# Optimization experiments

Measured on AMD Instinct MI355X. Metric: run time of the kernel, lower is better.

Reference implementation:

```python
import jax, jax.numpy as jnp
import numpy as np

DIM = 512

def setup_inputs() -> dict:
    key = jax.random.key(0)
    ks = jax.random.split(key, 8)
    B, T, S, D = 4, 128, 512, DIM
    scale = 1.0 / np.sqrt(D)
    return {
        "inp": jax.random.normal(ks[0], (B, T, D), jnp.float32),
        "context": jax.random.normal(ks[1], (B, S, D), jnp.float32),
        # linear_query: Linear(D, D, bias=True)
        "Wq": jax.random.normal(ks[2], (D, D), jnp.float32) * scale,
        "bq": jax.random.normal(ks[3], (D,), jnp.float32) * scale,
        # linear_context: Linear(D, D, bias=False)
        "Wc": jax.random.normal(ks[4], (D, D), jnp.float32) * scale,
        # v: Linear(D, 1, bias=False)
        "v": jax.random.normal(ks[5], (D,), jnp.float32) * scale,
        # linear_out: Linear(2D, D, bias=True)
        "Wout": jax.random.normal(ks[6], (D, 2 * D), jnp.float32) * scale,
        "bout": jax.random.normal(ks[7], (D,), jnp.float32) * scale,
    }

def reference(inp, context, Wq, bq, Wc, v, Wout, bout):
    # inp: (B,T,D) target queries; context: (B,S,D) source states
    wq = jnp.einsum('btd,ed->bte', inp, Wq) + bq          # (B,T,D)
    uh = jnp.einsum('bsd,ed->bse', context, Wc)            # (B,S,D)
    # additive (Bahdanau) score: v^T tanh(Wq q_t + Wc h_s)
    wquh = jnp.tanh(wq[:, :, None, :] + uh[:, None, :, :])  # (B,T,S,D)
    align = jnp.einsum('btsd,d->bts', wquh, v)             # (B,T,S)
    align_vectors = jax.nn.softmax(align, axis=-1)          # softmax over src_len
    c = jnp.einsum('bts,bsd->btd', align_vectors, context)  # context vector
    concat_c = jnp.concatenate([c, inp], axis=-1)           # (B,T,2D)
    attn_h = jnp.einsum('btf,ef->bte', concat_c, Wout) + bout  # (B,T,D)
    return attn_h, align_vectors
```

## Files before the change

### kernel.cpp

```cpp
#include <hip/hip_runtime.h>
#include <hip/hip_bf16.h>
#include <math.h>


typedef __attribute__((ext_vector_type(8))) short short8;
typedef __attribute__((ext_vector_type(4))) float f32x4;
typedef unsigned short ushort_t;

static __device__ __forceinline__ unsigned short f2bf(float x) {
    union { __hip_bfloat16 h; unsigned short u; } c;
    c.h = __float2bfloat16(x);
    return c.u;
}
static __device__ __forceinline__ int bf2x(float lo, float hi) {
    return (int)(((unsigned)f2bf(hi) << 16) | (unsigned)f2bf(lo));
}

template<bool BF>
static __device__ __forceinline__ void load16(const void* base, size_t elemoff,
                                              int4& r0, int4& r1) {
    if (BF) {
        const int4* p = (const int4*)((const ushort_t*)base + elemoff);
        r0 = p[0]; r1 = p[1];
    } else {
        const float4* p = (const float4*)((const float*)base + elemoff);
        float4 a = p[0], b = p[1], c = p[2], d = p[3];
        r0.x = bf2x(a.x, a.y); r0.y = bf2x(a.z, a.w);
        r0.z = bf2x(b.x, b.y); r0.w = bf2x(b.z, b.w);
        r1.x = bf2x(c.x, c.y); r1.y = bf2x(c.z, c.w);
        r1.z = bf2x(d.x, d.y); r1.w = bf2x(d.z, d.w);
    }
}

template<bool A_BF, bool W_BF, int EPI>
static __device__ __forceinline__ void gemm_body(
    ushort_t* As, ushort_t* Ws,
    const void* A, const void* W, const float* bias,
    void* Cv, int K, int lda, int ldw, int ldc, int bm, int bn)
{
    const int tid = threadIdx.x;
    const int wave = tid >> 6, lane = tid & 63;
    const int mh = (wave & 1) * 32, nh = (wave >> 1) * 32;
    const int quad = lane >> 4, l16 = lane & 15;
    const int srow = tid >> 2, schunk = tid & 3;

    const size_t aoff = (size_t)(bm + srow) * lda + schunk * 16;
    const size_t woff = (size_t)(bn + srow) * ldw + schunk * 16;
    int4* AsW = (int4*)&As[srow * 72 + schunk * 16];
    int4* WsW = (int4*)&Ws[srow * 72 + schunk * 16];

    f32x4 acc00 = {0.f, 0.f, 0.f, 0.f}, acc01 = acc00, acc10 = acc00, acc11 = acc00;

    int4 a0r, a1r, w0r, w1r;
    load16<A_BF>(A, aoff, a0r, a1r);
    load16<W_BF>(W, woff, w0r, w1r);

    for (int k0 = 0; k0 < K; k0 += 64) {
        AsW[0] = a0r; AsW[1] = a1r;
        WsW[0] = w0r; WsW[1] = w1r;
        __syncthreads();
        if (k0 + 64 < K) {
            load16<A_BF>(A, aoff + k0 + 64, a0r, a1r);
            load16<W_BF>(W, woff + k0 + 64, w0r, w1r);
        }
        #pragma unroll
        for (int kk = 0; kk < 64; kk += 32) {
            short8 a0 = *(const short8*)&As[(mh + l16) * 72 + kk + quad * 8];
            short8 a1 = *(const short8*)&As[(mh + 16 + l16) * 72 + kk + quad * 8];
            short8 b0 = *(const short8*)&Ws[(nh + l16) * 72 + kk + quad * 8];
            short8 b1 = *(const short8*)&Ws[(nh + 16 + l16) * 72 + kk + quad * 8];
            acc00 = __builtin_amdgcn_mfma_f32_16x16x32_bf16(a0, b0, acc00, 0, 0, 0);
            acc01 = __builtin_amdgcn_mfma_f32_16x16x32_bf16(a0, b1, acc01, 0, 0, 0);
            acc10 = __builtin_amdgcn_mfma_f32_16x16x32_bf16(a1, b0, acc10, 0, 0, 0);
            acc11 = __builtin_amdgcn_mfma_f32_16x16x32_bf16(a1, b1, acc11, 0, 0, 0);
        }
        __syncthreads();
    }

    const int col0 = bn + nh + l16;
    const int col1 = col0 + 16;
    float bias0 = bias ? bias[col0] : 0.f;
    float bias1 = bias ? bias[col1] : 0.f;

    f32x4 accs[2][2] = {{acc00, acc01}, {acc10, acc11}};
    #pragma unroll
    for (int mt = 0; mt < 2; ++mt) {
        #pragma unroll
        for (int r = 0; r < 4; ++r) {
            int row = bm + mh + mt * 16 + quad * 4 + r;
            size_t rowoff = (size_t)row * ldc;
            float v0 = accs[mt][0][r] + bias0;
            float v1 = accs[mt][1][r] + bias1;
            if (EPI == 1) { v0 = __expf(2.f * v0); v1 = __expf(2.f * v1); }
            if (EPI == 2) {
                ushort_t* C = (ushort_t*)Cv;
                C[rowoff + col0] = f2bf(v0);
                C[rowoff + col1] = f2bf(v1);
            } else {
                float* C = (float*)Cv;
                C[rowoff + col0] = v0;
                C[rowoff + col1] = v1;
            }
        }
    }
}

__global__ __launch_bounds__(256) void fused_front(
    const float* __restrict__ inp, const float* __restrict__ ctx,
    const float* __restrict__ Wq, const float* __restrict__ bq,
    const float* __restrict__ Wc, const float* __restrict__ Wout,
    const float* __restrict__ bout,
    float* __restrict__ Ew, float* __restrict__ Eu, float* __restrict__ Y0,
    ushort_t* __restrict__ GT)
{
    __shared__ ushort_t As[64 * 72];
    __shared__ ushort_t Ws[64 * 72];
    const int bid = blockIdx.x;

    if (bid < 64) {
        gemm_body<false, false, 1>(As, Ws, inp, Wq, bq, Ew,
                                   512, 512, 512, 512, (bid & 7) * 64, (bid >> 3) * 64);
    } else if (bid < 320) {
        int i = bid - 64;
        gemm_body<false, false, 1>(As, Ws, ctx, Wc, nullptr, Eu,
                                   512, 512, 512, 512, (i & 31) * 64, (i >> 5) * 64);
    } else if (bid < 576) {
        int i = bid - 320;
        int b = i >> 6, j = i & 63;
        gemm_body<false, false, 2>(As, Ws, Wout, ctx + (size_t)b * 262144, nullptr,
                                   GT + (size_t)b * 262144,
                                   512, 1024, 512, 512, (j & 7) * 64, (j >> 3) * 64);
    } else {
        int i = bid - 576;
        gemm_body<false, false, 0>(As, Ws, inp, Wout + 512, bout, Y0,
                                   512, 512, 1024, 512, (i & 7) * 64, (i >> 3) * 64);
    }
}

__global__ __launch_bounds__(256) void align_kernel(
    const float* __restrict__ Ew, const float* __restrict__ Eu,
    const float* __restrict__ v, float* __restrict__ out)
{
    const int lane = threadIdx.x & 63, wave = threadIdx.x >> 6;
    const int b = blockIdx.z;
    const int t0 = blockIdx.y * 8 + wave * 2;
    const int s0 = blockIdx.x * 8;

    const float* w0p = Ew + (((size_t)(b * 128 + t0)) << 9);
    const float* w1p = w0p + 512;
    const float* up  = Eu + (((size_t)(b * 512 + s0)) << 9);

    float acc0[8], acc1[8];
    #pragma unroll
    for (int j = 0; j < 8; ++j) { acc0[j] = 0.f; acc1[j] = 0.f; }
    float vsum = 0.f;

    for (int k0 = 0; k0 < 512; k0 += 64) {
        float vk = v[k0 + lane];
        vsum += vk;
        float w0 = w0p[k0 + lane];
        float w1 = w1p[k0 + lane];
        #pragma unroll
        for (int j = 0; j < 8; ++j) {
            float u = up[((size_t)j << 9) + k0 + lane];
            float d0 = fmaf(w0, u, 1.f);
            float d1 = fmaf(w1, u, 1.f);
            float r0 = __builtin_amdgcn_rcpf(d0);
            float r1 = __builtin_amdgcn_rcpf(d1);
            acc0[j] = fmaf(vk, r0, acc0[j]);
            acc1[j] = fmaf(vk, r1, acc1[j]);
        }
    }

    float V = vsum;
    #pragma unroll
    for (int off = 32; off; off >>= 1) V += __shfl_xor(V, off, 64);

    float r0 = 0.f, r1 = 0.f;
    #pragma unroll
    for (int j = 0; j < 8; ++j) {
        float a = acc0[j], c = acc1[j];
        #pragma unroll
        for (int off = 32; off; off >>= 1) {
            a += __shfl_xor(a, off, 64);
            c += __shfl_xor(c, off, 64);
        }
        if (lane == j) { r0 = fmaf(-2.f, a, V); r1 = fmaf(-2.f, c, V); }
    }
    if (lane < 8) {
        size_t o = (((size_t)(b * 128 + t0)) << 9) + s0 + lane;
        out[o] = r0;
        out[o + 512] = r1;
    }
}

__global__ __launch_bounds__(256) void gemm_att(
    const float* __restrict__ Sraw, const ushort_t* __restrict__ GT,
    const float* __restrict__ Y0, float* __restrict__ attn,
    float* __restrict__ alignv)
{
    __shared__ ushort_t As[64 * 72];
    __shared__ ushort_t Ws[64 * 72];
    const int tid = threadIdx.x;
    const int b = blockIdx.z;
    const int bm = blockIdx.x * 64;
    const int bn = blockIdx.y * 64;
    const int wave = tid >> 6, lane = tid & 63;
    const int mh = (wave & 1) * 32, nh = (wave >> 1) * 32;
    const int quad = lane >> 4, l16 = lane & 15;
    const int srow = tid >> 2, schunk = tid & 3;

    const float* Srow = Sraw + (((size_t)(b * 128 + bm + srow)) << 9);

    const float4* qv = (const float4*)(Srow + schunk * 128);
    float mloc = -3.4e38f;
    #pragma unroll
    for (int i = 0; i < 32; ++i) {
        float4 x = qv[i];
        mloc = fmaxf(mloc, fmaxf(fmaxf(x.x, x.y), fmaxf(x.z, x.w)));
    }
    mloc = fmaxf(mloc, __shfl_xor(mloc, 1, 64));
    mloc = fmaxf(mloc, __shfl_xor(mloc, 2, 64));
    float ssum = 0.f;
    #pragma unroll
    for (int i = 0; i < 32; ++i) {
        float4 x = qv[i];
        ssum += __expf(x.x - mloc) + __expf(x.y - mloc)
              + __expf(x.z - mloc) + __expf(x.w - mloc);
    }
    ssum += __shfl_xor(ssum, 1, 64);
    ssum += __shfl_xor(ssum, 2, 64);
    const float rinv = __builtin_amdgcn_rcpf(ssum);

    const bool wr = (blockIdx.y == 0);
    float* arow = alignv + (((size_t)(b * 128 + bm + srow)) << 9);
    const ushort_t* GTb = GT + (size_t)b * 262144;
    const size_t woff = (size_t)(bn + srow) * 512 + schunk * 16;
    int4* AsW = (int4*)&As[srow * 72 + schunk * 16];
    int4* WsW = (int4*)&Ws[srow * 72 + schunk * 16];

    f32x4 acc00 = {0.f, 0.f, 0.f, 0.f}, acc01 = acc00, acc10 = acc00, acc11 = acc00;

    for (int k0 = 0; k0 < 512; k0 += 64) {
        const float4* ap = (const float4*)(Srow + k0 + schunk * 16);
        float4 x0 = ap[0], x1 = ap[1], x2 = ap[2], x3 = ap[3];
        float4 p0, p1, p2, p3;
        p0.x = __expf(x0.x - mloc) * rinv; p0.y = __expf(x0.y - mloc) * rinv;
        p0.z = __expf(x0.z - mloc) * rinv; p0.w = __expf(x0.w - mloc) * rinv;
        p1.x = __expf(x1.x - mloc) * rinv; p1.y = __expf(x1.y - mloc) * rinv;
        p1.z = __expf(x1.z - mloc) * rinv; p1.w = __expf(x1.w - mloc) * rinv;
        p2.x = __expf(x2.x - mloc) * rinv; p2.y = __expf(x2.y - mloc) * rinv;
        p2.z = __expf(x2.z - mloc) * rinv; p2.w = __expf(x2.w - mloc) * rinv;
        p3.x = __expf(x3.x - mloc) * rinv; p3.y = __expf(x3.y - mloc) * rinv;
        p3.z = __expf(x3.z - mloc) * rinv; p3.w = __expf(x3.w - mloc) * rinv;
        int4 w0r, w1r;
        load16<true>(GTb, woff + k0, w0r, w1r);
        if (wr) {
            float4* d = (float4*)(arow + k0 + schunk * 16);
            d[0] = p0; d[1] = p1; d[2] = p2; d[3] = p3;
        }
        int4 a0r, a1r;
        a0r.x = bf2x(p0.x, p0.y); a0r.y = bf2x(p0.z, p0.w);
        a0r.z = bf2x(p1.x, p1.y); a0r.w = bf2x(p1.z, p1.w);
        a1r.x = bf2x(p2.x, p2.y); a1r.y = bf2x(p2.z, p2.w);
        a1r.z = bf2x(p3.x, p3.y); a1r.w = bf2x(p3.z, p3.w);
        __syncthreads();
        AsW[0] = a0r; AsW[1] = a1r;
        WsW[0] = w0r; WsW[1] = w1r;
        __syncthreads();
        #pragma unroll
        for (int kk = 0; kk < 64; kk += 32) {
            short8 a0 = *(const short8*)&As[(mh + l16) * 72 + kk + quad * 8];
            short8 a1 = *(const short8*)&As[(mh + 16 + l16) * 72 + kk + quad * 8];
            short8 b0 = *(const short8*)&Ws[(nh + l16) * 72 + kk + quad * 8];
            short8 b1 = *(const short8*)&Ws[(nh + 16 + l16) * 72 + kk + quad * 8];
            acc00 = __builtin_amdgcn_mfma_f32_16x16x32_bf16(a0, b0, acc00, 0, 0, 0);
            acc01 = __builtin_amdgcn_mfma_f32_16x16x32_bf16(a0, b1, acc01, 0, 0, 0);
            acc10 = __builtin_amdgcn_mfma_f32_16x16x32_bf16(a1, b0, acc10, 0, 0, 0);
            acc11 = __builtin_amdgcn_mfma_f32_16x16x32_bf16(a1, b1, acc11, 0, 0, 0);
        }
    }

    const int col0 = bn + nh + l16;
    const int col1 = col0 + 16;
    f32x4 accs[2][2] = {{acc00, acc01}, {acc10, acc11}};
    #pragma unroll
    for (int mt = 0; mt < 2; ++mt) {
        #pragma unroll
        for (int r = 0; r < 4; ++r) {
            size_t rowoff = (size_t)(b * 128 + bm + mh + mt * 16 + quad * 4 + r) << 9;
            attn[rowoff + col0] = accs[mt][0][r] + Y0[rowoff + col0];
            attn[rowoff + col1] = accs[mt][1][r] + Y0[rowoff + col1];
        }
    }
}

extern "C" void kernel_launch(void* const* d_in, const int* in_sizes, int n_in,
                              void* d_out, int out_size, void* d_ws, size_t ws_size,
                              hipStream_t stream)
{
    const float* inp  = (const float*)d_in[0];
    const float* ctx  = (const float*)d_in[1];
    const float* Wq   = (const float*)d_in[2];
    const float* bq   = (const float*)d_in[3];
    const float* Wc   = (const float*)d_in[4];
    const float* v    = (const float*)d_in[5];
    const float* Wout = (const float*)d_in[6];
    const float* bout = (const float*)d_in[7];

    float* out   = (float*)d_out;
    float* attn  = out;
    float* align = out + 262144;

    float* ws = (float*)d_ws;
    float* Ew   = ws;
    float* Eu   = ws + 262144;
    float* Y0   = ws + 1310720;
    float* Sraw = ws + 1572864;
    ushort_t* GT = (ushort_t*)(ws + 1835008);

    fused_front<<<dim3(640), 256, 0, stream>>>(inp, ctx, Wq, bq, Wc, Wout, bout,
                                               Ew, Eu, Y0, GT);
    align_kernel<<<dim3(64, 16, 4), 256, 0, stream>>>(Ew, Eu, v, Sraw);
    gemm_att<<<dim3(2, 8, 4), 256, 0, stream>>>(Sraw, GT, Y0, attn, align);
}
```

Measured before the change: 127.6 us.

## Fuse three kernels into one persistent kernel with grid barriers

Result: slower. 294.4 us (+130.6%).

```diff
diff --git a/kernel.cpp b/kernel.cpp
--- a/kernel.cpp
+++ b/kernel.cpp
@@ -56,6 +56,7 @@
     load16<W_BF>(W, woff, w0r, w1r);
 
     for (int k0 = 0; k0 < K; k0 += 64) {
+        __syncthreads();
         AsW[0] = a0r; AsW[1] = a1r;
         WsW[0] = w0r; WsW[1] = w1r;
         __syncthreads();
@@ -74,7 +75,6 @@
             acc10 = __builtin_amdgcn_mfma_f32_16x16x32_bf16(a1, b0, acc10, 0, 0, 0);
             acc11 = __builtin_amdgcn_mfma_f32_16x16x32_bf16(a1, b1, acc11, 0, 0, 0);
         }
-        __syncthreads();
     }
 
     const int col0 = bn + nh + l16;
@@ -105,46 +105,41 @@
     }
 }
 
-__global__ __launch_bounds__(256) void fused_front(
-    const float* __restrict__ inp, const float* __restrict__ ctx,
-    const float* __restrict__ Wq, const float* __restrict__ bq,
-    const float* __restrict__ Wc, const float* __restrict__ Wout,
-    const float* __restrict__ bout,
-    float* __restrict__ Ew, float* __restrict__ Eu, float* __restrict__ Y0,
-    ushort_t* __restrict__ GT)
-{
-    __shared__ ushort_t As[64 * 72];
-    __shared__ ushort_t Ws[64 * 72];
-    const int bid = blockIdx.x;
-
-    if (bid < 64) {
+static __device__ __forceinline__ void front_tile(
+    int t, ushort_t* As, ushort_t* Ws,
+    const float* inp, const float* ctx, const float* Wq, const float* bq,
+    const float* Wc, const float* Wout, const float* bout,
+    float* Ew, float* Eu, float* Y0, ushort_t* GT)
+{
+    if (t < 64) {
         gemm_body<false, false, 1>(As, Ws, inp, Wq, bq, Ew,
-                                   512, 512, 512, 512, (bid & 7) * 64, (bid >> 3) * 64);
-    } else if (bid < 320) {
-        int i = bid - 64;
+                                   512, 512, 512, 512, (t & 7) * 64, (t >> 3) * 64);
+    } else if (t < 320) {
+        int i = t - 64;
         gemm_body<false, false, 1>(As, Ws, ctx, Wc, nullptr, Eu,
                                    512, 512, 512, 512, (i & 31) * 64, (i >> 5) * 64);
-    } else if (bid < 576) {
-        int i = bid - 320;
+    } else if (t < 576) {
+        int i = t - 320;
         int b = i >> 6, j = i & 63;
         gemm_body<false, false, 2>(As, Ws, Wout, ctx + (size_t)b * 262144, nullptr,
                                    GT + (size_t)b * 262144,
                                    512, 1024, 512, 512, (j & 7) * 64, (j >> 3) * 64);
     } else {
-        int i = bid - 576;
+        int i = t - 576;
         gemm_body<false, false, 0>(As, Ws, inp, Wout + 512, bout, Y0,
                                    512, 512, 1024, 512, (i & 7) * 64, (i >> 3) * 64);
     }
 }
 
-__global__ __launch_bounds__(256) void align_kernel(
-    const float* __restrict__ Ew, const float* __restrict__ Eu,
-    const float* __restrict__ v, float* __restrict__ out)
+static __device__ __forceinline__ void align_tile(
+    int idx, const float* Ew, const float* Eu, const float* v, float* out)
 {
     const int lane = threadIdx.x & 63, wave = threadIdx.x >> 6;
-    const int b = blockIdx.z;
-    const int t0 = blockIdx.y * 8 + wave * 2;
-    const int s0 = blockIdx.x * 8;
+    const int sx = idx & 63;
+    const int ty = (idx >> 6) & 15;
+    const int b  = idx >> 10;
+    const int t0 = ty * 8 + wave * 2;
+    const int s0 = sx * 8;
 
     const float* w0p = Ew + (((size_t)(b * 128 + t0)) << 9);
     const float* w1p = w0p + 512;
@@ -194,17 +189,14 @@
     }
 }
 
-__global__ __launch_bounds__(256) void gemm_att(
-    const float* __restrict__ Sraw, const ushort_t* __restrict__ GT,
-    const float* __restrict__ Y0, float* __restrict__ attn,
-    float* __restrict__ alignv)
-{
-    __shared__ ushort_t As[64 * 72];
-    __shared__ ushort_t Ws[64 * 72];
+static __device__ __forceinline__ void att_tile(
+    int idx, ushort_t* As, ushort_t* Ws,
+    const float* Sraw, const ushort_t* GT, const float* Y0,
+    float* attn, float* alignv)
+{
+    const int bx = idx & 1, by = (idx >> 1) & 7, b = idx >> 4;
     const int tid = threadIdx.x;
-    const int b = blockIdx.z;
-    const int bm = blockIdx.x * 64;
-    const int bn = blockIdx.y * 64;
+    const int bm = bx * 64, bn = by * 64;
     const int wave = tid >> 6, lane = tid & 63;
     const int mh = (wave & 1) * 32, nh = (wave >> 1) * 32;
     const int quad = lane >> 4, l16 = lane & 15;
@@ -232,7 +224,7 @@
     ssum += __shfl_xor(ssum, 2, 64);
     const float rinv = __builtin_amdgcn_rcpf(ssum);
 
-    const bool wr = (blockIdx.y == 0);
+    const bool wr = (by == 0);
     float* arow = alignv + (((size_t)(b * 128 + bm + srow)) << 9);
     const ushort_t* GTb = GT + (size_t)b * 262144;
     const size_t woff = (size_t)(bn + srow) * 512 + schunk * 16;
@@ -295,6 +287,45 @@
     }
 }
 
+static __device__ __forceinline__ void grid_barrier(int* bar, int target) {
+    __syncthreads();
+    if (threadIdx.x == 0) {
+        __threadfence();
+        __hip_atomic_fetch_add(bar, 1, __ATOMIC_ACQ_REL, __HIP_MEMORY_SCOPE_AGENT);
+        while (__hip_atomic_load(bar, __ATOMIC_ACQUIRE, __HIP_MEMORY_SCOPE_AGENT) < target)
+            __builtin_amdgcn_s_sleep(2);
+        __threadfence();
+    }
+    __syncthreads();
+}
+
+__global__ __launch_bounds__(256, 4) void mega(
+    const float* __restrict__ inp, const float* __restrict__ ctx,
+    const float* __restrict__ Wq, const float* __restrict__ bq,
+    const float* __restrict__ Wc, const float* __restrict__ v,
+    const float* __restrict__ Wout, const float* __restrict__ bout,
+    float* __restrict__ Ew, float* __restrict__ Eu, float* __restrict__ Y0,
+    ushort_t* __restrict__ GT, float* __restrict__ Sraw,
+    float* __restrict__ attn, float* __restrict__ alignv, int* bar)
+{
+    __shared__ ushort_t As[64 * 72];
+    __shared__ ushort_t Ws[64 * 72];
+    const int nblk = gridDim.x;
+
+    for (int t = blockIdx.x; t < 640; t += nblk)
+        front_tile(t, As, Ws, inp, ctx, Wq, bq, Wc, Wout, bout, Ew, Eu, Y0, GT);
+
+    grid_barrier(bar, nblk);
+
+    for (int i = blockIdx.x; i < 4096; i += nblk)
+        align_tile(i, Ew, Eu, v, Sraw);
+
+    grid_barrier(bar, 2 * nblk);
+
+    for (int i = blockIdx.x; i < 64; i += nblk)
+        att_tile(i, As, Ws, Sraw, GT, Y0, attn, alignv);
+}
+
 extern "C" void kernel_launch(void* const* d_in, const int* in_sizes, int n_in,
                               void* d_out, int out_size, void* d_ws, size_t ws_size,
                               hipStream_t stream)
@@ -308,9 +339,9 @@
     const float* Wout = (const float*)d_in[6];
     const float* bout = (const float*)d_in[7];
 
-    float* out   = (float*)d_out;
-    float* attn  = out;
-    float* align = out + 262144;
+    float* out    = (float*)d_out;
+    float* attn   = out;
+    float* alignv = out + 262144;
 
     float* ws = (float*)d_ws;
     float* Ew   = ws;
@@ -318,9 +349,16 @@
     float* Y0   = ws + 1310720;
     float* Sraw = ws + 1572864;
     ushort_t* GT = (ushort_t*)(ws + 1835008);
-
-    fused_front<<<dim3(640), 256, 0, stream>>>(inp, ctx, Wq, bq, Wc, Wout, bout,
-                                               Ew, Eu, Y0, GT);
-    align_kernel<<<dim3(64, 16, 4), 256, 0, stream>>>(Ew, Eu, v, Sraw);
-    gemm_att<<<dim3(2, 8, 4), 256, 0, stream>>>(Sraw, GT, Y0, attn, align);
-}
+    int* bar = (int*)(ws + 2359296);
+
+    int maxB = 1;
+    if (hipOccupancyMaxActiveBlocksPerMultiprocessor(&maxB, mega, 256, 0) != hipSuccess
+        || maxB < 1)
+        maxB = 1;
+    if (maxB > 4) maxB = 4;
+    int nblk = 256 * maxB;
+
+    hipMemsetAsync(bar, 0, 256, stream);
+    mega<<<dim3(nblk), 256, 0, stream>>>(inp, ctx, Wq, bq, Wc, v, Wout, bout,
+                                         Ew, Eu, Y0, GT, Sraw, attn, alignv, bar);
+}
```
